# Kernel optimization log

Measured on AMD Instinct MI355X. Metric: run time of the kernel, lower is better.

Reference implementation:

```python
import jax, jax.numpy as jnp
import numpy as np

D_MODEL = 768
NUM_HEADS = 12
NUM_REG = 4
EPS = 1e-5


def _layernorm(x, g, b):
    mu = jnp.mean(x, axis=-1, keepdims=True)
    var = jnp.mean(jnp.square(x - mu), axis=-1, keepdims=True)
    return (x - mu) * jax.lax.rsqrt(var + EPS) * g + b


def _make_mask(seq_len):
    # True = masked (disallowed), matching torch attn_mask bool semantics.
    r1 = 1 + NUM_REG
    mask = np.ones((seq_len, seq_len), dtype=bool)
    mask[0, :] = False                      # context token attends to all
    mask[1:r1, :] = False                   # register tokens attend to all
    mask[r1:, :r1] = False                  # (not use_input_context_token) == False
    mask[r1:, r1:] = ~np.eye(seq_len - r1, dtype=bool)  # feature tokens: self only
    return jnp.asarray(mask)


def setup_inputs() -> dict:
    key = jax.random.key(0)
    ks = jax.random.split(key, 16)
    B, C, H, W = 8, D_MODEL, 32, 32
    d = D_MODEL
    s = 0.02
    inp = {
        "x": jax.random.normal(ks[0], (B, C, H, W), jnp.float32),
        "context_token": jax.random.normal(ks[1], (B, 1, d), jnp.float32),
        "register_tokens": jax.random.normal(ks[2], (B, NUM_REG, d), jnp.float32),
        "in_proj_w": jax.random.normal(ks[3], (3 * d, d), jnp.float32) * s,
        "in_proj_b": jnp.zeros((3 * d,), jnp.float32),
        "out_w": jax.random.normal(ks[4], (d, d), jnp.float32) * s,
        "out_b": jnp.zeros((d,), jnp.float32),
        "ln1_g": jnp.ones((d,), jnp.float32),
        "ln1_b": jnp.zeros((d,), jnp.float32),
        "ln2_g": jnp.ones((d,), jnp.float32),
        "ln2_b": jnp.zeros((d,), jnp.float32),
        "w1": jax.random.normal(ks[5], (4 * d, d), jnp.float32) * s,
        "b1": jnp.zeros((4 * d,), jnp.float32),
        "w2": jax.random.normal(ks[6], (d, 4 * d), jnp.float32) * s,
        "b2": jnp.zeros((d,), jnp.float32),
    }
    return inp


def reference(x, context_token, register_tokens, in_proj_w, in_proj_b,
              out_w, out_b, ln1_g, ln1_b, ln2_g, ln2_b, w1, b1, w2, b2):
    B, C, H, W = x.shape
    d, nh = D_MODEL, NUM_HEADS
    hd = d // nh
    x_flat = x.reshape(B, C, H * W).transpose(0, 2, 1)          # [B, HW, d]
    tokens = jnp.concatenate([context_token, register_tokens], axis=1)
    xw = _layernorm(jnp.concatenate([tokens, x_flat], axis=1), ln1_g, ln1_b)  # [B, S, d]
    S = xw.shape[1]

    qkv = xw @ in_proj_w.T + in_proj_b                           # [B, S, 3d]
    q, k, v = jnp.split(qkv, 3, axis=-1)
    q = q.reshape(B, S, nh, hd).transpose(0, 2, 1, 3)            # [B, nh, S, hd]
    k = k.reshape(B, S, nh, hd).transpose(0, 2, 1, 3)
    v = v.reshape(B, S, nh, hd).transpose(0, 2, 1, 3)

    scores = jnp.einsum("bhqd,bhkd->bhqk", q, k) / jnp.sqrt(jnp.float32(hd))
    mask = _make_mask(S)
    scores = jnp.where(mask, jnp.float32(-1e9), scores)
    probs = jax.nn.softmax(scores, axis=-1)
    attn = jnp.einsum("bhqk,bhkd->bhqd", probs, v)               # [B, nh, S, hd]
    attn = attn.transpose(0, 2, 1, 3).reshape(B, S, d)
    attn = attn @ out_w.T + out_b

    h1 = attn + xw                                                # residual
    ff = _layernorm(h1, ln2_g, ln2_b)
    ff = jax.nn.gelu(ff @ w1.T + b1, approximate=False) @ w2.T + b2
    out = ff + h1                                                 # [B, S, d]

    r1 = 1 + NUM_REG
    ctx_out = out[:, 0:1, :]
    reg_out = out[:, 1:r1, :]
    feat_out = out[:, r1:, :].transpose(0, 2, 1).reshape(B, C, H, W)
    return feat_out, ctx_out, reg_out
```

## Files before the change

### kernel.cpp

```cpp
#include <hip/hip_runtime.h>
#include <math.h>
#include <stdint.h>

#define SEQ 1029
#define BATCH 8
#define M_TOT (BATCH * SEQ)
#define M_PAD 8320
#define NCHUNK 17

typedef float floatx4 __attribute__((ext_vector_type(4)));
typedef __bf16 bf16x8 __attribute__((ext_vector_type(8)));

__device__ __forceinline__ unsigned short f2bf(float f) {
  union { float f; unsigned u; } v; v.f = f;
  unsigned r = v.u + 0x7fffu + ((v.u >> 16) & 1u);
  return (unsigned short)(r >> 16);
}
__device__ __forceinline__ float bf2f(unsigned short h) {
  union { unsigned u; float f; } v; v.u = ((unsigned)h) << 16;
  return v.f;
}
__device__ __forceinline__ float bf_lo(unsigned u) { union { unsigned x; float f; } v; v.x = u << 16; return v.f; }
__device__ __forceinline__ float bf_hi(unsigned u) { union { unsigned x; float f; } v; v.x = u & 0xffff0000u; return v.f; }

__device__ __forceinline__ float wave_sum(float v) {
#pragma unroll
  for (int off = 32; off > 0; off >>= 1) v += __shfl_xor(v, off, 64);
  return v;
}
__device__ __forceinline__ float wave_max(float v) {
#pragma unroll
  for (int off = 32; off > 0; off >>= 1) v = fmaxf(v, __shfl_xor(v, off, 64));
  return v;
}

__device__ __forceinline__ void gload16(const unsigned short* g, unsigned short* l) {
  __builtin_amdgcn_global_load_lds(
      (const __attribute__((address_space(1))) unsigned int*)g,
      (__attribute__((address_space(3))) unsigned int*)l, 16, 0, 0);
}

#define NQ_QKV 442368
#define NQ_OUT 147456
#define NQ_W1  589824
#define NQ_W2  589824
#define NQ_PAD 8448
__global__ void convert_all(const float4* __restrict__ inw, const float4* __restrict__ outw,
                            const float4* __restrict__ w1, const float4* __restrict__ w2,
                            ushort4* __restrict__ wqkv, ushort4* __restrict__ wout,
                            ushort4* __restrict__ w1b, ushort4* __restrict__ w2b,
                            ushort4* __restrict__ xw_pad, ushort4* __restrict__ attn_pad) {
  const int i = blockIdx.x * 256 + threadIdx.x;
  const float4* src; ushort4* dst; int off;
  if (i < NQ_QKV) { src = inw; dst = wqkv; off = i; }
  else if (i < NQ_QKV + NQ_OUT) { src = outw; dst = wout; off = i - NQ_QKV; }
  else if (i < NQ_QKV + NQ_OUT + NQ_W1) { src = w1; dst = w1b; off = i - NQ_QKV - NQ_OUT; }
  else if (i < NQ_QKV + NQ_OUT + NQ_W1 + NQ_W2) { src = w2; dst = w2b; off = i - NQ_QKV - NQ_OUT - NQ_W1; }
  else {
    const int j = i - (NQ_QKV + NQ_OUT + NQ_W1 + NQ_W2);
    const ushort4 z = {0, 0, 0, 0};
    if (j < NQ_PAD) { xw_pad[j] = z; attn_pad[j] = z; }
    return;
  }
  const float4 v = src[off];
  ushort4 o;
  o.x = f2bf(v.x); o.y = f2bf(v.y); o.z = f2bf(v.z); o.w = f2bf(v.w);
  dst[off] = o;
}
#define NQ_ALL (NQ_QKV + NQ_OUT + NQ_W1 + NQ_W2 + NQ_PAD)

__global__ __launch_bounds__(256) void ln1_feat(const float* __restrict__ x,
                                                const float* __restrict__ g,
                                                const float* __restrict__ bta,
                                                unsigned short* __restrict__ xw) {
  __shared__ float tile[768 * 17];
  const int b = blockIdx.y;
  const int hw0 = blockIdx.x * 16;
  const int t = threadIdx.x;
  const float* xb = x + (size_t)b * 768 * 1024;
  const int cl = t >> 4, hl = t & 15;
  for (int it = 0; it < 48; it++) {
    const int c = it * 16 + cl;
    tile[c * 17 + hl] = xb[(size_t)c * 1024 + hw0 + hl];
  }
  __syncthreads();
  const int wave = t >> 6, lane = t & 63;
  for (int tk = wave; tk < 16; tk += 4) {
    float vals[12], s = 0.f, ss = 0.f;
#pragma unroll
    for (int i = 0; i < 12; i++) {
      const float v = tile[(lane + 64 * i) * 17 + tk];
      vals[i] = v; s += v; ss += v * v;
    }
    s = wave_sum(s); ss = wave_sum(ss);
    const float mu = s * (1.0f / 768.0f);
    const float var = ss * (1.0f / 768.0f) - mu * mu;
    const float rs = rsqrtf(var + 1e-5f);
    const int row = b * SEQ + 5 + hw0 + tk;
    unsigned short* orow = xw + (size_t)row * 768;
#pragma unroll
    for (int i = 0; i < 12; i++) {
      const int c = lane + 64 * i;
      orow[c] = f2bf((vals[i] - mu) * rs * g[c] + bta[c]);
    }
  }
}

__global__ __launch_bounds__(256) void ln1_special(const float* __restrict__ ctx,
                                                   const float* __restrict__ regs,
                                                   const float* __restrict__ g,
                                                   const float* __restrict__ bta,
                                                   unsigned short* __restrict__ xw) {
  const int gw = blockIdx.x * 4 + (threadIdx.x >> 6);
  const int lane = threadIdx.x & 63;
  if (gw >= 40) return;
  const int b = gw / 5, s = gw % 5;
  const float* src = (s == 0) ? (ctx + (size_t)b * 768)
                              : (regs + ((size_t)b * 4 + (s - 1)) * 768);
  float vals[12], sm = 0.f, ss = 0.f;
#pragma unroll
  for (int i = 0; i < 12; i++) {
    const float v = src[lane + 64 * i];
    vals[i] = v; sm += v; ss += v * v;
  }
  sm = wave_sum(sm); ss = wave_sum(ss);
  const float mu = sm * (1.0f / 768.0f);
  const float var = ss * (1.0f / 768.0f) - mu * mu;
  const float rs = rsqrtf(var + 1e-5f);
  unsigned short* orow = xw + (size_t)(b * SEQ + s) * 768;
#pragma unroll
  for (int i = 0; i < 12; i++) {
    const int c = lane + 64 * i;
    orow[c] = f2bf((vals[i] - mu) * rs * g[c] + bta[c]);
  }
}

#define BM 128
#define BN 128
#define BK 32

template <int EPI, int K, int N>
__global__ __launch_bounds__(256, 4) void gemm_bt(const unsigned short* __restrict__ A,
                                                  const unsigned short* __restrict__ W,
                                                  const float* __restrict__ bias,
                                                  const unsigned short* __restrict__ residb,
                                                  const float* __restrict__ residf,
                                                  float* __restrict__ outf,
                                                  unsigned short* __restrict__ outb) {
  __shared__ alignas(16) unsigned short As[2][BM * BK];
  __shared__ alignas(16) unsigned short Ws[2][BN * BK];
  const int t = threadIdx.x;
  const int wave = t >> 6, lane = t & 63;
  const int quad = lane >> 4, l16 = lane & 15;
  const int wm = (wave & 1) * 64, wn = (wave >> 1) * 64;
  const int tileM = blockIdx.y * BM, tileN = blockIdx.x * BN;

  const int rl = lane >> 2;
  const int kc8 = ((lane & 3) ^ ((rl >> 1) & 3)) * 8;
  const unsigned short* Ag = A + (size_t)(tileM + wave * 16 + rl) * K;
  const unsigned short* Wg = W + (size_t)(tileN + wave * 16 + rl) * K;
  const int ldst = wave * 512 + lane * 8;

  const int koff = ((quad ^ ((l16 >> 1) & 3)) * 8);

  const floatx4 zero4 = {0.f, 0.f, 0.f, 0.f};
  floatx4 acc[4][4];
#pragma unroll
  for (int i = 0; i < 4; i++)
#pragma unroll
    for (int j = 0; j < 4; j++) acc[i][j] = zero4;

  auto dma = [&](int k0, int buf) {
    gload16(Ag + k0 + kc8, &As[buf][0] + ldst);
    gload16(Ag + (size_t)64 * K + k0 + kc8, &As[buf][0] + ldst + 2048);
    gload16(Wg + k0 + kc8, &Ws[buf][0] + ldst);
    gload16(Wg + (size_t)64 * K + k0 + kc8, &Ws[buf][0] + ldst + 2048);
  };
  auto compute = [&](int buf) {
    bf16x8 af[4], wf[4];
#pragma unroll
    for (int i = 0; i < 4; i++)
      af[i] = *(const bf16x8*)(&As[buf][0] + (wm + i * 16 + l16) * BK + koff);
#pragma unroll
    for (int j = 0; j < 4; j++)
      wf[j] = *(const bf16x8*)(&Ws[buf][0] + (wn + j * 16 + l16) * BK + koff);
#pragma unroll
    for (int i = 0; i < 4; i++)
#pragma unroll
      for (int j = 0; j < 4; j++)
        acc[i][j] = __builtin_amdgcn_mfma_f32_16x16x32_bf16(af[i], wf[j], acc[i][j], 0, 0, 0);
  };

  dma(0, 0);
#pragma unroll 1
  for (int k0 = 0; k0 < K; k0 += 2 * BK) {
    __syncthreads();
    if (k0 + BK < K) dma(k0 + BK, 1);
    compute(0);
    __syncthreads();
    if (k0 + 2 * BK < K) dma(k0 + 2 * BK, 0);
    compute(1);
  }

#pragma unroll
  for (int i = 0; i < 4; i++) {
    const int mbase = tileM + wm + i * 16 + quad * 4;
#pragma unroll
    for (int j = 0; j < 4; j++) {
      const int n = tileN + wn + j * 16 + l16;
      const float bv = bias[n];
#pragma unroll
      for (int r = 0; r < 4; r++) {
        const size_t idx = (size_t)(mbase + r) * N + n;
        float v = acc[i][j][r] + bv;
        if constexpr (EPI == 0) {
          outb[idx] = f2bf(v);
        } else if constexpr (EPI == 1) {
          outf[idx] = v + bf2f(residb[idx]);
        } else if constexpr (EPI == 2) {
          v = 0.5f * v * (1.0f + erff(v * 0.70710678118654752f));
          outb[idx] = f2bf(v);
        } else {
          outf[idx] = v + residf[idx];
        }
      }
    }
  }
}

__global__ __launch_bounds__(256) void attn_feat(const unsigned short* __restrict__ qkv,
                                                 unsigned short* __restrict__ attn) {
  __shared__ float kk[5][64];
  __shared__ float vv[5][64];
  const int b = blockIdx.z, h = blockIdx.y;
  const int t = threadIdx.x;
  const size_t base = (size_t)b * SEQ;
  for (int i = t; i < 320; i += 256) {
    const int j = i >> 6, dd = i & 63;
    const size_t rb = (base + j) * 2304 + (size_t)h * 64 + dd;
    kk[j][dd] = bf2f(qkv[rb + 768]);
    vv[j][dd] = bf2f(qkv[rb + 1536]);
  }
  __syncthreads();
  const int wave = t >> 6, lane = t & 63;
  const int s = 5 + blockIdx.x * 4 + wave;
  const size_t row = (base + s) * 2304 + (size_t)h * 64;
  const float q = bf2f(qkv[row + lane]);
  const float kself = bf2f(qkv[row + 768 + lane]);
  const float vself = bf2f(qkv[row + 1536 + lane]);
  float sc[6];
#pragma unroll
  for (int j = 0; j < 5; j++) sc[j] = wave_sum(q * kk[j][lane]) * 0.125f;
  sc[5] = wave_sum(q * kself) * 0.125f;
  float mx = sc[0];
#pragma unroll
  for (int j = 1; j < 6; j++) mx = fmaxf(mx, sc[j]);
  float den = 0.f, e[6];
#pragma unroll
  for (int j = 0; j < 6; j++) { e[j] = expf(sc[j] - mx); den += e[j]; }
  const float inv = 1.0f / den;
  float o = 0.f;
#pragma unroll
  for (int j = 0; j < 5; j++) o += e[j] * vv[j][lane];
  o += e[5] * vself;
  attn[(base + s) * 768 + (size_t)h * 64 + lane] = f2bf(o * inv);
}

__global__ __launch_bounds__(256) void attn_part(const unsigned short* __restrict__ qkv,
                                                 float* __restrict__ part) {
  __shared__ float qs[5][64];
  __shared__ float sc[5][64];
  __shared__ float mArr[5], lArr[5];
  __shared__ float og[4][320];
  const int c = blockIdx.x, h = blockIdx.y, b = blockIdx.z;
  const int t = threadIdx.x;
  const size_t base = (size_t)b * SEQ;
  const int kbase = (c < 16) ? (5 + 64 * c) : 0;
  const int nvalid = (c < 16) ? 64 : 5;

  for (int i = t; i < 320; i += 256)
    qs[i >> 6][i & 63] = bf2f(qkv[(base + (i >> 6)) * 2304 + (size_t)h * 64 + (i & 63)]);
  __syncthreads();

  const int keyloc = t >> 2, dc = t & 3;
  const int key = kbase + keyloc;
  const unsigned short* krow = qkv + (base + key) * 2304 + 768 + (size_t)h * 64;
  const uint4 k0 = *(const uint4*)(krow + dc * 8);
  const uint4 k1 = *(const uint4*)(krow + dc * 8 + 32);
  float kf[16];
  {
    const unsigned ku[8] = {k0.x, k0.y, k0.z, k0.w, k1.x, k1.y, k1.z, k1.w};
#pragma unroll
    for (int j = 0; j < 8; j++) { kf[2 * j] = bf_lo(ku[j]); kf[2 * j + 1] = bf_hi(ku[j]); }
  }
#pragma unroll
  for (int q = 0; q < 5; q++) {
    const float* qp = qs[q];
    float d0 = 0.f;
#pragma unroll
    for (int j = 0; j < 8; j++) d0 += qp[dc * 8 + j] * kf[j];
#pragma unroll
    for (int j = 0; j < 8; j++) d0 += qp[dc * 8 + 32 + j] * kf[8 + j];
    d0 += __shfl_xor(d0, 1, 64);
    d0 += __shfl_xor(d0, 2, 64);
    if (dc == 0) sc[q][keyloc] = (keyloc < nvalid) ? d0 * 0.125f : -1e30f;
  }
  __syncthreads();

  const int wave = t >> 6, lane = t & 63;
  for (int q = wave; q < 5; q += 4) {
    const float v = sc[q][lane];
    const float m = wave_max(v);
    const float e = expf(v - m);
    sc[q][lane] = e;
    const float l = wave_sum(e);
    if (lane == 0) { mArr[q] = m; lArr[q] = l; }
  }
  __syncthreads();

  const int d = t & 63, g = t >> 6;
  float o[5] = {0.f, 0.f, 0.f, 0.f, 0.f};
  for (int i = 0; i < 16; i++) {
    const int kl = g * 16 + i;
    const float v = bf2f(qkv[(base + kbase + kl) * 2304 + 1536 + (size_t)h * 64 + d]);
#pragma unroll
    for (int q = 0; q < 5; q++) o[q] += sc[q][kl] * v;
  }
#pragma unroll
  for (int q = 0; q < 5; q++) og[g][q * 64 + d] = o[q];
  __syncthreads();

  float* pw = part + (size_t)((b * 12 + h) * NCHUNK + c) * 5 * 66;
  for (int i = t; i < 320; i += 256) {
    const int q = i >> 6, dd = i & 63;
    pw[q * 66 + 2 + dd] = og[0][i] + og[1][i] + og[2][i] + og[3][i];
    if (dd == 0) { pw[q * 66] = mArr[q]; pw[q * 66 + 1] = lArr[q]; }
  }
}

__global__ __launch_bounds__(64) void attn_comb(const float* __restrict__ part,
                                                unsigned short* __restrict__ attn) {
  const int qi = blockIdx.x, h = blockIdx.y, b = blockIdx.z;
  const int d = threadIdx.x;
  float M = -3e38f, L = 0.f, o = 0.f;
  for (int c = 0; c < NCHUNK; c++) {
    const float* p = part + ((size_t)((b * 12 + h) * NCHUNK + c) * 5 + qi) * 66;
    const float mc = p[0], lc = p[1], oc = p[2 + d];
    if (mc > M) {
      const float s = expf(M - mc);
      L = L * s + lc; o = o * s + oc; M = mc;
    } else {
      const float w = expf(mc - M);
      L += lc * w; o += oc * w;
    }
  }
  attn[((size_t)b * SEQ + qi) * 768 + (size_t)h * 64 + d] = f2bf(o / L);
}

__global__ __launch_bounds__(256) void ln2_kernel(const float* __restrict__ h1,
                                                  const float* __restrict__ g,
                                                  const float* __restrict__ bta,
                                                  unsigned short* __restrict__ out) {
  const int row = blockIdx.x * 4 + (threadIdx.x >> 6);
  const int lane = threadIdx.x & 63;
  const float* r = h1 + (size_t)row * 768;
  float vals[12], sm = 0.f, ss = 0.f;
#pragma unroll
  for (int i = 0; i < 12; i++) {
    const float v = r[lane + 64 * i];
    vals[i] = v; sm += v; ss += v * v;
  }
  sm = wave_sum(sm); ss = wave_sum(ss);
  const float mu = sm * (1.0f / 768.0f);
  const float var = ss * (1.0f / 768.0f) - mu * mu;
  const float rs = rsqrtf(var + 1e-5f);
  unsigned short* orow = out + (size_t)row * 768;
#pragma unroll
  for (int i = 0; i < 12; i++) {
    const int c = lane + 64 * i;
    orow[c] = f2bf((vals[i] - mu) * rs * g[c] + bta[c]);
  }
}

__global__ __launch_bounds__(256) void scatter_all(const float* __restrict__ outb,
                                                   float* __restrict__ dout) {
  const int t = threadIdx.x;
  const int b = blockIdx.z;
  if (blockIdx.x == 24) {
    const int i = (b * 32 + blockIdx.y) * 256 + t;
    if (i >= 40 * 768) return;
    const int rowi = i / 768, c = i % 768;
    const int bb = rowi / 5, s = rowi % 5;
    const float v = outb[(size_t)(bb * SEQ + s) * 768 + c];
    if (s == 0) dout[6291456 + (size_t)bb * 768 + c] = v;
    else dout[6291456 + 6144 + ((size_t)bb * 4 + (s - 1)) * 768 + c] = v;
    return;
  }
  __shared__ float tl[32][33];
  const int hw0 = blockIdx.y * 32, c0 = blockIdx.x * 32;
  const int i = t >> 5, j = t & 31;
#pragma unroll
  for (int r = 0; r < 4; r++) {
    const int hwi = i + r * 8;
    tl[hwi][j] = outb[(size_t)(b * SEQ + 5 + hw0 + hwi) * 768 + c0 + j];
  }
  __syncthreads();
#pragma unroll
  for (int r = 0; r < 4; r++) {
    const int ci = i + r * 8;
    dout[(size_t)b * 768 * 1024 + (size_t)(c0 + ci) * 1024 + hw0 + j] = tl[j][ci];
  }
}

extern "C" void kernel_launch(void* const* d_in, const int* in_sizes, int n_in,
                              void* d_out, int out_size, void* d_ws, size_t ws_size,
                              hipStream_t stream) {
  const float* x    = (const float*)d_in[0];
  const float* ctx  = (const float*)d_in[1];
  const float* regs = (const float*)d_in[2];
  const float* inw  = (const float*)d_in[3];
  const float* inb  = (const float*)d_in[4];
  const float* outw = (const float*)d_in[5];
  const float* outbi= (const float*)d_in[6];
  const float* ln1g = (const float*)d_in[7];
  const float* ln1b = (const float*)d_in[8];
  const float* ln2g = (const float*)d_in[9];
  const float* ln2b = (const float*)d_in[10];
  const float* w1   = (const float*)d_in[11];
  const float* b1   = (const float*)d_in[12];
  const float* w2   = (const float*)d_in[13];
  const float* b2   = (const float*)d_in[14];

  char* ws = (char*)d_ws;
  unsigned short* wqkv_b = (unsigned short*)(ws + 0);
  unsigned short* wout_b = (unsigned short*)(ws + 3538944);
  unsigned short* w1_b   = (unsigned short*)(ws + 4718592);
  unsigned short* w2_b   = (unsigned short*)(ws + 9437184);
  unsigned short* xw_b   = (unsigned short*)(ws + 14155776);
  unsigned short* ln2o_b = (unsigned short*)(ws + 26935296);
  float*          h1_f   = (float*)(ws + 39714816);
  unsigned short* qkv_b  = (unsigned short*)(ws + 65273856);
  unsigned short* attn_b = (unsigned short*)(ws + 103612416);
  float*          out_f  = (float*)(ws + 14155776);
  unsigned short* ffm_b  = (unsigned short*)(ws + 65273856);
  float*          part_f = (float*)(ws + 39714816);
  float* dout = (float*)d_out;

  convert_all<<<(NQ_ALL + 255) / 256, 256, 0, stream>>>(
      (const float4*)inw, (const float4*)outw, (const float4*)w1, (const float4*)w2,
      (ushort4*)wqkv_b, (ushort4*)wout_b, (ushort4*)w1_b, (ushort4*)w2_b,
      (ushort4*)(xw_b + (size_t)M_TOT * 768), (ushort4*)(attn_b + (size_t)M_TOT * 768));

  ln1_feat<<<dim3(64, 8), 256, 0, stream>>>(x, ln1g, ln1b, xw_b);
  ln1_special<<<10, 256, 0, stream>>>(ctx, regs, ln1g, ln1b, xw_b);

  gemm_bt<0, 768, 2304><<<dim3(2304 / BN, M_PAD / BM), 256, 0, stream>>>(
      xw_b, wqkv_b, inb, nullptr, nullptr, nullptr, qkv_b);

  attn_feat<<<dim3(256, 12, 8), 256, 0, stream>>>(qkv_b, attn_b);
  attn_part<<<dim3(NCHUNK, 12, 8), 256, 0, stream>>>(qkv_b, part_f);
  attn_comb<<<dim3(5, 12, 8), 64, 0, stream>>>(part_f, attn_b);

  gemm_bt<1, 768, 768><<<dim3(768 / BN, M_PAD / BM), 256, 0, stream>>>(
      attn_b, wout_b, outbi, xw_b, nullptr, h1_f, nullptr);

  ln2_kernel<<<M_PAD / 4, 256, 0, stream>>>(h1_f, ln2g, ln2b, ln2o_b);

  gemm_bt<2, 768, 3072><<<dim3(3072 / BN, M_PAD / BM), 256, 0, stream>>>(
      ln2o_b, w1_b, b1, nullptr, nullptr, nullptr, ffm_b);

  gemm_bt<3, 3072, 768><<<dim3(768 / BN, M_PAD / BM), 256, 0, stream>>>(
      ffm_b, w2_b, b2, nullptr, h1_f, out_f, nullptr);

  scatter_all<<<dim3(25, 32, 8), 256, 0, stream>>>(out_f, dout);
}
```

Baseline: 426.7 us.

## Remap GEMM tiles across XCDs and use 64-row tiles for N=768 GEMMs

The GEMM kernel now runs on a 1D grid. Block indices are remapped so that every N-tile of a given M row-tile runs on the same XCD (blockIdx.x & 7), which is meant to improve L2 reuse of the A operand. A template parameter MT selects the M-tile height, and the two GEMMs with N=768 (out-proj and FFN down-proj) switch to 64-row tiles. This doubles their tile count to reduce wave-quantization and idle CUs on the wide machine. The cost is some blocks that exit early as padding, plus lower per-block arithmetic intensity for the smaller tiles.

```diff
diff --git a/kernel.cpp b/kernel.cpp
--- a/kernel.cpp
+++ b/kernel.cpp
@@ -135,11 +135,10 @@
   }
 }
 
-#define BM 128
 #define BN 128
 #define BK 32
 
-template <int EPI, int K, int N>
+template <int EPI, int K, int N, int MT, int NM, int NN>
 __global__ __launch_bounds__(256, 4) void gemm_bt(const unsigned short* __restrict__ A,
                                                   const unsigned short* __restrict__ W,
                                                   const float* __restrict__ bias,
@@ -147,13 +146,20 @@
                                                   const float* __restrict__ residf,
                                                   float* __restrict__ outf,
                                                   unsigned short* __restrict__ outb) {
-  __shared__ alignas(16) unsigned short As[2][BM * BK];
+  constexpr int BMt = MT * 32;
+  __shared__ alignas(16) unsigned short As[2][BMt * BK];
   __shared__ alignas(16) unsigned short Ws[2][BN * BK];
+  const int xcd = blockIdx.x & 7;
+  const int slot = blockIdx.x >> 3;
+  const int tmIdx = xcd + 8 * (slot / NN);
+  const int tn = slot % NN;
+  if (tmIdx >= NM) return;
+  const int tileM = tmIdx * BMt, tileN = tn * BN;
+
   const int t = threadIdx.x;
   const int wave = t >> 6, lane = t & 63;
   const int quad = lane >> 4, l16 = lane & 15;
-  const int wm = (wave & 1) * 64, wn = (wave >> 1) * 64;
-  const int tileM = blockIdx.y * BM, tileN = blockIdx.x * BN;
+  const int wm = (wave & 1) * (MT * 16), wn = (wave >> 1) * 64;
 
   const int rl = lane >> 2;
   const int kc8 = ((lane & 3) ^ ((rl >> 1) & 3)) * 8;
@@ -164,28 +170,29 @@
   const int koff = ((quad ^ ((l16 >> 1) & 3)) * 8);
 
   const floatx4 zero4 = {0.f, 0.f, 0.f, 0.f};
-  floatx4 acc[4][4];
-#pragma unroll
-  for (int i = 0; i < 4; i++)
+  floatx4 acc[MT][4];
+#pragma unroll
+  for (int i = 0; i < MT; i++)
 #pragma unroll
     for (int j = 0; j < 4; j++) acc[i][j] = zero4;
 
   auto dma = [&](int k0, int buf) {
     gload16(Ag + k0 + kc8, &As[buf][0] + ldst);
-    gload16(Ag + (size_t)64 * K + k0 + kc8, &As[buf][0] + ldst + 2048);
+    if constexpr (MT == 4)
+      gload16(Ag + (size_t)64 * K + k0 + kc8, &As[buf][0] + ldst + 2048);
     gload16(Wg + k0 + kc8, &Ws[buf][0] + ldst);
     gload16(Wg + (size_t)64 * K + k0 + kc8, &Ws[buf][0] + ldst + 2048);
   };
   auto compute = [&](int buf) {
-    bf16x8 af[4], wf[4];
-#pragma unroll
-    for (int i = 0; i < 4; i++)
+    bf16x8 af[MT], wf[4];
+#pragma unroll
+    for (int i = 0; i < MT; i++)
       af[i] = *(const bf16x8*)(&As[buf][0] + (wm + i * 16 + l16) * BK + koff);
 #pragma unroll
     for (int j = 0; j < 4; j++)
       wf[j] = *(const bf16x8*)(&Ws[buf][0] + (wn + j * 16 + l16) * BK + koff);
 #pragma unroll
-    for (int i = 0; i < 4; i++)
+    for (int i = 0; i < MT; i++)
 #pragma unroll
       for (int j = 0; j < 4; j++)
         acc[i][j] = __builtin_amdgcn_mfma_f32_16x16x32_bf16(af[i], wf[j], acc[i][j], 0, 0, 0);
@@ -203,7 +210,7 @@
   }
 
 #pragma unroll
-  for (int i = 0; i < 4; i++) {
+  for (int i = 0; i < MT; i++) {
     const int mbase = tileM + wm + i * 16 + quad * 4;
 #pragma unroll
     for (int j = 0; j < 4; j++) {
@@ -454,22 +461,22 @@
   ln1_feat<<<dim3(64, 8), 256, 0, stream>>>(x, ln1g, ln1b, xw_b);
   ln1_special<<<10, 256, 0, stream>>>(ctx, regs, ln1g, ln1b, xw_b);
 
-  gemm_bt<0, 768, 2304><<<dim3(2304 / BN, M_PAD / BM), 256, 0, stream>>>(
+  gemm_bt<0, 768, 2304, 4, 65, 18><<<8 * 9 * 18, 256, 0, stream>>>(
       xw_b, wqkv_b, inb, nullptr, nullptr, nullptr, qkv_b);
 
   attn_feat<<<dim3(256, 12, 8), 256, 0, stream>>>(qkv_b, attn_b);
   attn_part<<<dim3(NCHUNK, 12, 8), 256, 0, stream>>>(qkv_b, part_f);
   attn_comb<<<dim3(5, 12, 8), 64, 0, stream>>>(part_f, attn_b);
 
-  gemm_bt<1, 768, 768><<<dim3(768 / BN, M_PAD / BM), 256, 0, stream>>>(
+  gemm_bt<1, 768, 768, 2, 130, 6><<<8 * 17 * 6, 256, 0, stream>>>(
       attn_b, wout_b, outbi, xw_b, nullptr, h1_f, nullptr);
 
   ln2_kernel<<<M_PAD / 4, 256, 0, stream>>>(h1_f, ln2g, ln2b, ln2o_b);
 
-  gemm_bt<2, 768, 3072><<<dim3(3072 / BN, M_PAD / BM), 256, 0, stream>>>(
+  gemm_bt<2, 768, 3072, 4, 65, 24><<<8 * 9 * 24, 256, 0, stream>>>(
       ln2o_b, w1_b, b1, nullptr, nullptr, nullptr, ffm_b);
 
-  gemm_bt<3, 3072, 768><<<dim3(768 / BN, M_PAD / BM), 256, 0, stream>>>(
+  gemm_bt<3, 3072, 768, 2, 130, 6><<<8 * 17 * 6, 256, 0, stream>>>(
       ffm_b, w2_b, b2, nullptr, h1_f, out_f, nullptr);
 
   scatter_all<<<dim3(25, 32, 8), 256, 0, stream>>>(out_f, dout);
```

Measured after the change: 428.3 us. Within noise of the previous version (+0.4%).
